# Optimization experiments

Hardware: AMD Instinct MI355X
Metric: run time of the kernel (lower is better)

Reference implementation:

```python
import jax, jax.numpy as jnp
import numpy as np

N = 50000      # nodes
E = 800000     # edges (before self loops)
F = 128        # node_feat_dim
HID = 128      # hidden_dim
LN_EPS = 1e-5
NEG_SLOPE = 0.2


def setup_inputs() -> dict:
    key = jax.random.key(0)
    ks = jax.random.split(key, 32)
    g = lambda k, shape, s=0.05: jax.random.normal(k, shape, dtype=jnp.float32) * s
    inp = {}
    inp["x"] = jax.random.normal(ks[0], (N, F), dtype=jnp.float32)
    inp["edge_index"] = jax.random.randint(ks[1], (2, E), 0, N)
    i = 2
    # conv1: F -> 4 heads x 32, concat -> HID
    inp["W1l"] = g(ks[i], (F, HID)); inp["b1l"] = jnp.zeros((HID,), jnp.float32)
    inp["W1r"] = g(ks[i+1], (F, HID)); inp["b1r"] = jnp.zeros((HID,), jnp.float32)
    inp["a1"] = g(ks[i+2], (4, HID // 4)); inp["c1"] = jnp.zeros((HID,), jnp.float32)
    inp["g1"] = jnp.ones((HID,), jnp.float32); inp["be1"] = jnp.zeros((HID,), jnp.float32)
    # conv2: HID -> 4 heads x 32, concat -> HID
    inp["W2l"] = g(ks[i+3], (HID, HID)); inp["b2l"] = jnp.zeros((HID,), jnp.float32)
    inp["W2r"] = g(ks[i+4], (HID, HID)); inp["b2r"] = jnp.zeros((HID,), jnp.float32)
    inp["a2"] = g(ks[i+5], (4, HID // 4)); inp["c2"] = jnp.zeros((HID,), jnp.float32)
    inp["g2"] = jnp.ones((HID,), jnp.float32); inp["be2"] = jnp.zeros((HID,), jnp.float32)
    # conv3: HID -> 1 head x HID, mean -> HID
    inp["W3l"] = g(ks[i+6], (HID, HID)); inp["b3l"] = jnp.zeros((HID,), jnp.float32)
    inp["W3r"] = g(ks[i+7], (HID, HID)); inp["b3r"] = jnp.zeros((HID,), jnp.float32)
    inp["a3"] = g(ks[i+8], (1, HID)); inp["c3"] = jnp.zeros((HID,), jnp.float32)
    inp["g3"] = jnp.ones((HID,), jnp.float32); inp["be3"] = jnp.zeros((HID,), jnp.float32)
    return inp


def _gatv2(x, Wl, bl, Wr, br, att, bias, src, dst, heads, outc, concat):
    """GATv2Conv: xl=source transform, xr=target transform, edge-wise
    LeakyReLU attention, per-destination segment softmax, scatter-add."""
    n = x.shape[0]
    xl = (x @ Wl + bl).reshape(n, heads, outc)   # lin_l -> source (x_j)
    e_feat = jax.nn.leaky_relu(xl[src] + ((x @ Wr + br).reshape(n, heads, outc))[dst], NEG_SLOPE)  # [E,H,C]
    logits = jnp.einsum('ehc,hc->eh', e_feat, att)                 # [E,H]
    m = jax.ops.segment_max(logits, dst, num_segments=n)           # [N,H]
    a = jnp.exp(logits - m[dst])
    denom = jax.ops.segment_sum(a, dst, num_segments=n)            # [N,H]
    a = a / denom[dst]
    out = jax.ops.segment_sum(xl[src] * a[:, :, None], dst, num_segments=n)  # [N,H,C]
    out = out.reshape(n, heads * outc) if concat else out.mean(axis=1)
    return out + bias


def _ln(h, g, b):
    mu = h.mean(-1, keepdims=True)
    var = ((h - mu) ** 2).mean(-1, keepdims=True)
    return (h - mu) * jax.lax.rsqrt(var + LN_EPS) * g + b


def reference(x, edge_index,
              W1l, b1l, W1r, b1r, a1, c1, g1, be1,
              W2l, b2l, W2r, b2r, a2, c2, g2, be2,
              W3l, b3l, W3r, b3r, a3, c3, g3, be3):
    n = x.shape[0]
    loops = jnp.arange(n, dtype=edge_index.dtype)
    src = jnp.concatenate([edge_index[0], loops])  # add_self_loops=True
    dst = jnp.concatenate([edge_index[1], loops])
    h = _gatv2(x, W1l, b1l, W1r, b1r, a1, c1, src, dst, 4, HID // 4, True)
    h = jax.nn.relu(_ln(h, g1, be1))  # dropout is identity in eval
    h = _gatv2(h, W2l, b2l, W2r, b2r, a2, c2, src, dst, 4, HID // 4, True)
    h = jax.nn.relu(_ln(h, g2, be2))
    h = _gatv2(h, W3l, b3l, W3r, b3r, a3, c3, src, dst, 1, HID, False)
    h = jax.nn.relu(_ln(h, g3, be3))
    return h
```

## Files before the change

kernel.cpp:

```cpp
#include <hip/hip_runtime.h>
#include <hip/hip_bf16.h>


typedef __attribute__((ext_vector_type(8))) short bf16x8;
typedef __attribute__((ext_vector_type(4))) float f32x4;
typedef __attribute__((ext_vector_type(2))) float f32x2;

#define CAP 64

__device__ __forceinline__ ushort f2bf(float f) {
    unsigned u = __float_as_uint(f);
    unsigned r = (u + 0x7fffu + ((u >> 16) & 1u)) >> 16;
    return (ushort)r;
}
__device__ __forceinline__ f32x2 up2(unsigned u) {
    f32x2 r;
    r[0] = __uint_as_float(u << 16);
    r[1] = __uint_as_float(u & 0xffff0000u);
    return r;
}


__global__ __launch_bounds__(256) void prep_kernel(
    const float* __restrict__ x, ushort* __restrict__ xb, int n4,
    const float* W0, const float* W1, const float* W2,
    const float* W3, const float* W4, const float* W5,
    ushort* __restrict__ WT) {
    __shared__ ushort s[128 * 129];
    int tid = threadIdx.x;
    if (blockIdx.x < 6) {
        const float* Ws[6] = {W0, W1, W2, W3, W4, W5};
        const float* W = Ws[blockIdx.x];
        ushort* O = WT + blockIdx.x * 16384;
        for (int r = 0; r < 128; r += 2) {
            int k = r + (tid >> 7);
            int nn = tid & 127;
            s[nn * 129 + k] = f2bf(W[k * 128 + nn]);
        }
        __syncthreads();
        for (int i = tid; i < 16384; i += 256) {
            int nn = i >> 7, k = i & 127;
            O[i] = s[nn * 129 + k];
        }
    } else {
        int i = (blockIdx.x - 6) * 256 + tid;
        if (i >= n4) return;
        float4 v = ((const float4*)x)[i];
        ushort4 o;
        o.x = f2bf(v.x); o.y = f2bf(v.y); o.z = f2bf(v.z); o.w = f2bf(v.w);
        ((ushort4*)xb)[i] = o;
    }
}


__global__ __launch_bounds__(256) void scatter_part_kernel(
    const int* __restrict__ srcrow, const int* __restrict__ dstrow,
    int E, int n, int* __restrict__ cursor, int* __restrict__ srcs) {
    int part = blockIdx.x & 7;
    int sub = blockIdx.x >> 3;
    int nsub = gridDim.x >> 3;
    int ppn = (n + 7) / 8;
    int lo = part * ppn;
    int hi = lo + ppn; if (hi > n) hi = n;
    int ET = E + n;
    int chunk = (ET + nsub - 1) / nsub;
    int s0 = sub * chunk, s1 = s0 + chunk; if (s1 > ET) s1 = ET;
    for (int i = s0 + threadIdx.x; i < s1; i += 256) {
        int d = (i < E) ? dstrow[i] : (i - E);
        if (d >= lo && d < hi) {
            int s = (i < E) ? srcrow[i] : (i - E);
            int pos = atomicAdd(&cursor[d], 1);
            if (pos < CAP) srcs[(d << 6) + pos] = s << 8;
        }
    }
}


__global__ __launch_bounds__(256) void dual_gemm_mfma(
    const ushort* __restrict__ A,
    const ushort* __restrict__ WTl, const ushort* __restrict__ WTr,
    const float* __restrict__ bl, const float* __restrict__ br,
    ushort* __restrict__ XL, ushort* __restrict__ XR, int n) {
    int tid = threadIdx.x;
    int wid = tid >> 6, lane = tid & 63;
    int ln15 = lane & 15, hi = lane >> 4;
    int row0 = blockIdx.x * 64;

    const ushort* WT  = (wid < 2) ? WTl : WTr;
    const float* bias = (wid < 2) ? bl : br;
    ushort* OUT       = (wid < 2) ? XL : XR;
    int colbase = (wid & 1) * 64;

    float bv[4];
    #pragma unroll
    for (int nn = 0; nn < 4; ++nn) bv[nn] = bias[colbase + nn * 16 + ln15];

    f32x4 acc[4][4];
    #pragma unroll
    for (int m = 0; m < 4; ++m)
        #pragma unroll
        for (int nn = 0; nn < 4; ++nn) acc[m][nn] = (f32x4){0.f, 0.f, 0.f, 0.f};

    #pragma unroll
    for (int kk = 0; kk < 4; ++kk) {
        int kb = kk * 64 + hi * 16;
        bf16x8 a[4], b[4];
        #pragma unroll
        for (int m = 0; m < 4; ++m) {
            int r = row0 + m * 16 + ln15;
            a[m] = *(const bf16x8*)((const char*)A + (size_t)r * 256 + kb);
        }
        #pragma unroll
        for (int nn = 0; nn < 4; ++nn) {
            int c = colbase + nn * 16 + ln15;
            b[nn] = *(const bf16x8*)((const char*)WT + (size_t)c * 256 + kb);
        }
        #pragma unroll
        for (int m = 0; m < 4; ++m)
            #pragma unroll
            for (int nn = 0; nn < 4; ++nn)
                acc[m][nn] = __builtin_amdgcn_mfma_f32_16x16x32_bf16(a[m], b[nn], acc[m][nn], 0, 0, 0);
    }

    #pragma unroll
    for (int m = 0; m < 4; ++m) {
        int rbase = row0 + m * 16 + hi * 4;
        bool full = (rbase + 3 < n);
        #pragma unroll
        for (int nn = 0; nn < 4; ++nn) {
            int c = colbase + nn * 16 + ln15;
            ushort* o = OUT + (size_t)rbase * 128 + c;
            float b = bv[nn];
            __hip_bfloat162 h01 = __float22bfloat162_rn(make_float2(acc[m][nn][0] + b, acc[m][nn][1] + b));
            __hip_bfloat162 h23 = __float22bfloat162_rn(make_float2(acc[m][nn][2] + b, acc[m][nn][3] + b));
            ushort2 u01 = *(ushort2*)&h01;
            ushort2 u23 = *(ushort2*)&h23;
            if (full) {
                o[0] = u01.x; o[128] = u01.y; o[256] = u23.x; o[384] = u23.y;
            } else {
                if (rbase + 0 < n) o[0]   = u01.x;
                if (rbase + 1 < n) o[128] = u01.y;
                if (rbase + 2 < n) o[256] = u23.x;
                if (rbase + 3 < n) o[384] = u23.y;
            }
        }
    }
}


template <int GS>
__device__ __forceinline__ void edge_op(uint4 U, const f32x2* xr, const f32x2* at,
                                        f32x2* acc, float& den) {
    f32x2 a0 = up2(U.x), a1 = up2(U.y), a2 = up2(U.z), a3 = up2(U.w);
    f32x2 t = a0 + xr[0];
    t = __builtin_elementwise_max(t, t * 0.2f);
    f32x2 dd = t * at[0];
    t = a1 + xr[1];
    t = __builtin_elementwise_max(t, t * 0.2f);
    dd = __builtin_elementwise_fma(t, at[1], dd);
    t = a2 + xr[2];
    t = __builtin_elementwise_max(t, t * 0.2f);
    dd = __builtin_elementwise_fma(t, at[2], dd);
    t = a3 + xr[3];
    t = __builtin_elementwise_max(t, t * 0.2f);
    dd = __builtin_elementwise_fma(t, at[3], dd);
    float p = dd[0] + dd[1];
    #pragma unroll
    for (int d = 1; d < GS; d <<= 1) p += __shfl_xor(p, d, 64);
    float ew = exp2f(p);
    f32x2 ev; ev[0] = ew; ev[1] = ew;
    acc[0] = __builtin_elementwise_fma(ev, a0, acc[0]);
    acc[1] = __builtin_elementwise_fma(ev, a1, acc[1]);
    acc[2] = __builtin_elementwise_fma(ev, a2, acc[2]);
    acc[3] = __builtin_elementwise_fma(ev, a3, acc[3]);
    den += ew;
}

template <int H, bool OUT_BF16>
__global__ __launch_bounds__(256) void aggregate_kernel(
    const ushort* __restrict__ XL, const ushort* __restrict__ XR,
    const int* __restrict__ deg, const int* __restrict__ srcs,
    const float* __restrict__ att, const float* __restrict__ bias,
    const float* __restrict__ gamma, const float* __restrict__ beta,
    void* __restrict__ OUTP, int n) {
    int tid = threadIdx.x;
    int wid = tid >> 6, lane = tid & 63;
    int g = lane >> 4, l = lane & 15;
    int node = blockIdx.x * 16 + wid * 4 + g;
    bool alive = (node < n);
    int c0 = l * 8;
    constexpr int GS = (128 / H) / 8;

    const char* XLc = (const char*)XL;
    int lb = l * 16;

    f32x2 at[4];
    {
        const float4* ap = (const float4*)(att + c0);
        float4 a0 = ap[0], a1 = ap[1];
        at[0][0] = a0.x; at[0][1] = a0.y; at[1][0] = a0.z; at[1][1] = a0.w;
        at[2][0] = a1.x; at[2][1] = a1.y; at[3][0] = a1.z; at[3][1] = a1.w;
        #pragma unroll
        for (int j = 0; j < 4; ++j) at[j] = at[j] * 1.44269504f;
    }

    f32x2 xr[4];
    int e = 0;
    const int* sp = srcs;
    if (alive) {
        uint4 ur = *(const uint4*)((const char*)XR + ((size_t)node << 8) + lb);
        xr[0] = up2(ur.x); xr[1] = up2(ur.y); xr[2] = up2(ur.z); xr[3] = up2(ur.w);
        e = deg[node]; if (e > CAP) e = CAP;
        sp = srcs + ((size_t)node << 6);
    } else {
        #pragma unroll
        for (int j = 0; j < 4; ++j) { xr[j][0] = 0.f; xr[j][1] = 0.f; }
    }

    f32x2 acc[4];
    #pragma unroll
    for (int j = 0; j < 4; ++j) { acc[j][0] = 0.f; acc[j][1] = 0.f; }
    float den = 0.f;

    int i = 0;
    for (; i + 4 <= e; i += 4) {
        int4 ofs = *(const int4*)(sp + i);
        uint4 u0 = *(const uint4*)(XLc + ofs.x + lb);
        uint4 u1 = *(const uint4*)(XLc + ofs.y + lb);
        uint4 u2 = *(const uint4*)(XLc + ofs.z + lb);
        uint4 u3 = *(const uint4*)(XLc + ofs.w + lb);
        edge_op<GS>(u0, xr, at, acc, den);
        edge_op<GS>(u1, xr, at, acc, den);
        edge_op<GS>(u2, xr, at, acc, den);
        edge_op<GS>(u3, xr, at, acc, den);
    }
    for (; i < e; ++i) {
        uint4 u0 = *(const uint4*)(XLc + sp[i] + lb);
        edge_op<GS>(u0, xr, at, acc, den);
    }

    float inv = 1.f / den;
    f32x2 o[4];
    {
        const f32x2* bp = (const f32x2*)(bias + c0);
        f32x2 iv; iv[0] = inv; iv[1] = inv;
        #pragma unroll
        for (int j = 0; j < 4; ++j) o[j] = __builtin_elementwise_fma(acc[j], iv, bp[j]);
    }

    float ssum = 0.f;
    #pragma unroll
    for (int j = 0; j < 4; ++j) ssum += o[j][0] + o[j][1];
    #pragma unroll
    for (int d = 1; d < 16; d <<= 1) ssum += __shfl_xor(ssum, d, 64);
    float mu = ssum * (1.f / 128.f);
    float vsum = 0.f;
    #pragma unroll
    for (int j = 0; j < 4; ++j) {
        float d0 = o[j][0] - mu, d1 = o[j][1] - mu;
        vsum += d0 * d0 + d1 * d1;
    }
    #pragma unroll
    for (int d = 1; d < 16; d <<= 1) vsum += __shfl_xor(vsum, d, 64);
    float rstd = rsqrtf(vsum * (1.f / 128.f) + 1e-5f);

    if (!alive) return;

    const f32x2* gp = (const f32x2*)(gamma + c0);
    const f32x2* ep = (const f32x2*)(beta + c0);
    float y[8];
    #pragma unroll
    for (int j = 0; j < 4; ++j) {
        f32x2 gj = gp[j], bj = ep[j];
        y[2 * j]     = fmaxf(fmaf((o[j][0] - mu) * rstd, gj[0], bj[0]), 0.f);
        y[2 * j + 1] = fmaxf(fmaf((o[j][1] - mu) * rstd, gj[1], bj[1]), 0.f);
    }

    if (OUT_BF16) {
        __hip_bfloat162 h0 = __float22bfloat162_rn(make_float2(y[0], y[1]));
        __hip_bfloat162 h1 = __float22bfloat162_rn(make_float2(y[2], y[3]));
        __hip_bfloat162 h2 = __float22bfloat162_rn(make_float2(y[4], y[5]));
        __hip_bfloat162 h3 = __float22bfloat162_rn(make_float2(y[6], y[7]));
        uint4 ov;
        ov.x = *(unsigned*)&h0; ov.y = *(unsigned*)&h1;
        ov.z = *(unsigned*)&h2; ov.w = *(unsigned*)&h3;
        *(uint4*)&((ushort*)OUTP)[(size_t)node * 128 + c0] = ov;
    } else {
        float* O = (float*)OUTP + (size_t)node * 128 + c0;
        *(float4*)O = make_float4(y[0], y[1], y[2], y[3]);
        *(float4*)(O + 4) = make_float4(y[4], y[5], y[6], y[7]);
    }
}


extern "C" void kernel_launch(void* const* d_in, const int* in_sizes, int n_in,
                              void* d_out, int out_size, void* d_ws, size_t ws_size,
                              hipStream_t stream) {
    const float* x  = (const float*)d_in[0];
    const int*   ei = (const int*)d_in[1];
    const float *W1l = (const float*)d_in[2],  *b1l = (const float*)d_in[3];
    const float *W1r = (const float*)d_in[4],  *b1r = (const float*)d_in[5];
    const float *a1  = (const float*)d_in[6],  *c1  = (const float*)d_in[7];
    const float *g1  = (const float*)d_in[8],  *be1 = (const float*)d_in[9];
    const float *W2l = (const float*)d_in[10], *b2l = (const float*)d_in[11];
    const float *W2r = (const float*)d_in[12], *b2r = (const float*)d_in[13];
    const float *a2  = (const float*)d_in[14], *c2  = (const float*)d_in[15];
    const float *g2  = (const float*)d_in[16], *be2 = (const float*)d_in[17];
    const float *W3l = (const float*)d_in[18], *b3l = (const float*)d_in[19];
    const float *W3r = (const float*)d_in[20], *b3r = (const float*)d_in[21];
    const float *a3  = (const float*)d_in[22], *c3  = (const float*)d_in[23];
    const float *g3  = (const float*)d_in[24], *be3 = (const float*)d_in[25];

    int n  = in_sizes[0] / 128;
    int E  = in_sizes[1] / 2;
    size_t nPad = (size_t)((n + 63) / 64) * 64;

    char* ws = (char*)d_ws;
    ushort* xb = (ushort*)ws;                      ws += nPad * 128 * 2;
    ushort* XL = (ushort*)ws;                      ws += nPad * 128 * 2;
    ushort* XR = (ushort*)ws;                      ws += nPad * 128 * 2;
    ushort* hb = (ushort*)ws;                      ws += nPad * 128 * 2;
    ushort* WT = (ushort*)ws;                      ws += 6 * 16384 * 2;
    int* cursor = (int*)ws;                        ws += (size_t)n * 4;
    int* srcs   = (int*)ws;

    const int* srcrow = ei;
    const int* dstrow = ei + E;

    int n4 = n * 128 / 4;
    prep_kernel<<<6 + (n4 + 255) / 256, 256, 0, stream>>>(
        x, xb, n4, W1l, W1r, W2l, W2r, W3l, W3r, WT);

    hipMemsetAsync(cursor, 0, (size_t)n * sizeof(int), stream);
    scatter_part_kernel<<<2048, 256, 0, stream>>>(srcrow, dstrow, E, n, cursor, srcs);

    int gb = (int)(nPad / 64);
    int ab = (n + 15) / 16;

    dual_gemm_mfma<<<gb, 256, 0, stream>>>(xb, WT + 0 * 16384, WT + 1 * 16384, b1l, b1r, XL, XR, n);
    aggregate_kernel<4, true><<<ab, 256, 0, stream>>>(XL, XR, cursor, srcs, a1, c1, g1, be1, hb, n);
    dual_gemm_mfma<<<gb, 256, 0, stream>>>(hb, WT + 2 * 16384, WT + 3 * 16384, b2l, b2r, XL, XR, n);
    aggregate_kernel<4, true><<<ab, 256, 0, stream>>>(XL, XR, cursor, srcs, a2, c2, g2, be2, hb, n);
    dual_gemm_mfma<<<gb, 256, 0, stream>>>(hb, WT + 4 * 16384, WT + 5 * 16384, b3l, b3r, XL, XR, n);
    aggregate_kernel<1, false><<<ab, 256, 0, stream>>>(XL, XR, cursor, srcs, a3, c3, g3, be3, d_out, n);
}
```

Before: 368.5 us.

## Split multi-head aggregation per head with node-range partitioning, separate LayerNorm pass

For the two 4-head layers, the fused aggregate+LayerNorm kernel is replaced by a per-head aggregation kernel. Each block handles one head over a contiguous node range, so every gather fetches only a 64-byte slice of XL. This is meant to shrink the gather working set per block and improve cache locality. A separate LayerNorm+ReLU kernel then runs in place on the bf16 output, which adds an extra read/write pass and a launch. The cursor memset is also folded into the prep kernel to drop one API call.

```diff
diff --git a/kernel.cpp b/kernel.cpp
--- a/kernel.cpp
+++ b/kernel.cpp
@@ -25,7 +25,7 @@
     const float* __restrict__ x, ushort* __restrict__ xb, int n4,
     const float* W0, const float* W1, const float* W2,
     const float* W3, const float* W4, const float* W5,
-    ushort* __restrict__ WT) {
+    ushort* __restrict__ WT, int* __restrict__ cursor, int nzb, int n) {
     __shared__ ushort s[128 * 129];
     int tid = threadIdx.x;
     if (blockIdx.x < 6) {
@@ -42,8 +42,16 @@
             int nn = i >> 7, k = i & 127;
             O[i] = s[nn * 129 + k];
         }
+    } else if (blockIdx.x < 6 + nzb) {
+        int base = (blockIdx.x - 6) * 1024 + tid * 4;
+        if (base + 3 < n) {
+            *(int4*)&cursor[base] = make_int4(0, 0, 0, 0);
+        } else {
+            for (int j = 0; j < 4; ++j)
+                if (base + j < n) cursor[base + j] = 0;
+        }
     } else {
-        int i = (blockIdx.x - 6) * 256 + tid;
+        int i = (blockIdx.x - 6 - nzb) * 256 + tid;
         if (i >= n4) return;
         float4 v = ((const float4*)x)[i];
         ushort4 o;
@@ -176,6 +184,153 @@
     den += ew;
 }
 
+
+__global__ __launch_bounds__(256) void agg_head_kernel(
+    const ushort* __restrict__ XL, const ushort* __restrict__ XR,
+    const int* __restrict__ deg, const int* __restrict__ srcs,
+    const float* __restrict__ att, const float* __restrict__ bias,
+    ushort* __restrict__ OUT, int n) {
+    int b = blockIdx.x;
+    int head = (b & 7) >> 1;
+    int s = ((b >> 3) << 1) | (b & 1);
+    int nsub = (gridDim.x >> 3) << 1;
+    int tid = threadIdx.x;
+    int wid = tid >> 6, lane = tid & 63;
+    int ng = lane >> 2;
+    int l4 = lane & 3;
+    int hb = head * 64 + l4 * 16;
+    int c0 = head * 32 + l4 * 8;
+
+    const char* XLc = (const char*)XL;
+
+    f32x2 at[4];
+    {
+        const float4* ap = (const float4*)(att + c0);
+        float4 a0 = ap[0], a1 = ap[1];
+        at[0][0] = a0.x; at[0][1] = a0.y; at[1][0] = a0.z; at[1][1] = a0.w;
+        at[2][0] = a1.x; at[2][1] = a1.y; at[3][0] = a1.z; at[3][1] = a1.w;
+        #pragma unroll
+        for (int j = 0; j < 4; ++j) at[j] = at[j] * 1.44269504f;
+    }
+    f32x2 bi[4];
+    {
+        const f32x2* bp = (const f32x2*)(bias + c0);
+        #pragma unroll
+        for (int j = 0; j < 4; ++j) bi[j] = bp[j];
+    }
+
+    int npb = (n + nsub - 1) / nsub;
+    int v0 = s * npb;
+    int v1 = v0 + npb; if (v1 > n) v1 = n;
+
+    for (int base = v0; base < v1; base += 64) {
+        int node = base + wid * 16 + ng;
+        bool alive = (node < v1);
+
+        f32x2 xr[4];
+        int e = 0;
+        const int* sp = srcs;
+        if (alive) {
+            uint4 ur = *(const uint4*)((const char*)XR + ((size_t)node << 8) + hb);
+            xr[0] = up2(ur.x); xr[1] = up2(ur.y); xr[2] = up2(ur.z); xr[3] = up2(ur.w);
+            e = deg[node]; if (e > CAP) e = CAP;
+            sp = srcs + ((size_t)node << 6);
+        } else {
+            #pragma unroll
+            for (int j = 0; j < 4; ++j) { xr[j][0] = 0.f; xr[j][1] = 0.f; }
+        }
+
+        f32x2 acc[4];
+        #pragma unroll
+        for (int j = 0; j < 4; ++j) { acc[j][0] = 0.f; acc[j][1] = 0.f; }
+        float den = 0.f;
+
+        int i = 0;
+        for (; i + 4 <= e; i += 4) {
+            int4 ofs = *(const int4*)(sp + i);
+            uint4 u0 = *(const uint4*)(XLc + ofs.x + hb);
+            uint4 u1 = *(const uint4*)(XLc + ofs.y + hb);
+            uint4 u2 = *(const uint4*)(XLc + ofs.z + hb);
+            uint4 u3 = *(const uint4*)(XLc + ofs.w + hb);
+            edge_op<4>(u0, xr, at, acc, den);
+            edge_op<4>(u1, xr, at, acc, den);
+            edge_op<4>(u2, xr, at, acc, den);
+            edge_op<4>(u3, xr, at, acc, den);
+        }
+        for (; i < e; ++i) {
+            uint4 u0 = *(const uint4*)(XLc + sp[i] + hb);
+            edge_op<4>(u0, xr, at, acc, den);
+        }
+
+        if (alive) {
+            float inv = 1.f / den;
+            f32x2 iv; iv[0] = inv; iv[1] = inv;
+            uint4 ov;
+            unsigned* op = (unsigned*)&ov;
+            #pragma unroll
+            for (int j = 0; j < 4; ++j) {
+                f32x2 o = __builtin_elementwise_fma(acc[j], iv, bi[j]);
+                __hip_bfloat162 h = __float22bfloat162_rn(make_float2(o[0], o[1]));
+                op[j] = *(unsigned*)&h;
+            }
+            *(uint4*)((char*)OUT + ((size_t)node << 8) + hb) = ov;
+        }
+    }
+}
+
+
+__global__ __launch_bounds__(256) void ln_relu_kernel(
+    ushort* __restrict__ H, const float* __restrict__ gamma,
+    const float* __restrict__ beta, int n) {
+    int tid = threadIdx.x;
+    int wid = tid >> 6, lane = tid & 63;
+    int node = blockIdx.x * 16 + wid * 4 + (lane >> 4);
+    int l = lane & 15, c0 = l * 8;
+    bool alive = (node < n);
+
+    f32x2 o[4];
+    if (alive) {
+        uint4 u = *(const uint4*)&H[(size_t)node * 128 + c0];
+        o[0] = up2(u.x); o[1] = up2(u.y); o[2] = up2(u.z); o[3] = up2(u.w);
+    } else {
+        #pragma unroll
+        for (int j = 0; j < 4; ++j) { o[j][0] = 0.f; o[j][1] = 0.f; }
+    }
+
+    float ssum = 0.f;
+    #pragma unroll
+    for (int j = 0; j < 4; ++j) ssum += o[j][0] + o[j][1];
+    #pragma unroll
+    for (int d = 1; d < 16; d <<= 1) ssum += __shfl_xor(ssum, d, 64);
+    float mu = ssum * (1.f / 128.f);
+    float vsum = 0.f;
+    #pragma unroll
+    for (int j = 0; j < 4; ++j) {
+        float d0 = o[j][0] - mu, d1 = o[j][1] - mu;
+        vsum += d0 * d0 + d1 * d1;
+    }
+    #pragma unroll
+    for (int d = 1; d < 16; d <<= 1) vsum += __shfl_xor(vsum, d, 64);
+    float rstd = rsqrtf(vsum * (1.f / 128.f) + 1e-5f);
+
+    if (!alive) return;
+
+    const f32x2* gp = (const f32x2*)(gamma + c0);
+    const f32x2* ep = (const f32x2*)(beta + c0);
+    uint4 ov;
+    unsigned* op = (unsigned*)&ov;
+    #pragma unroll
+    for (int j = 0; j < 4; ++j) {
+        f32x2 gj = gp[j], bj = ep[j];
+        float y0 = fmaxf(fmaf((o[j][0] - mu) * rstd, gj[0], bj[0]), 0.f);
+        float y1 = fmaxf(fmaf((o[j][1] - mu) * rstd, gj[1], bj[1]), 0.f);
+        __hip_bfloat162 h = __float22bfloat162_rn(make_float2(y0, y1));
+        op[j] = *(unsigned*)&h;
+    }
+    *(uint4*)&H[(size_t)node * 128 + c0] = ov;
+}
+
+
 template <int H, bool OUT_BF16>
 __global__ __launch_bounds__(256) void aggregate_kernel(
     const ushort* __restrict__ XL, const ushort* __restrict__ XR,
@@ -328,19 +483,21 @@
     const int* dstrow = ei + E;
 
     int n4 = n * 128 / 4;
-    prep_kernel<<<6 + (n4 + 255) / 256, 256, 0, stream>>>(
-        x, xb, n4, W1l, W1r, W2l, W2r, W3l, W3r, WT);
-
-    hipMemsetAsync(cursor, 0, (size_t)n * sizeof(int), stream);
+    int nzb = (n + 1023) / 1024;
+    prep_kernel<<<6 + nzb + (n4 + 255) / 256, 256, 0, stream>>>(
+        x, xb, n4, W1l, W1r, W2l, W2r, W3l, W3r, WT, cursor, nzb, n);
+
     scatter_part_kernel<<<2048, 256, 0, stream>>>(srcrow, dstrow, E, n, cursor, srcs);
 
     int gb = (int)(nPad / 64);
     int ab = (n + 15) / 16;
 
     dual_gemm_mfma<<<gb, 256, 0, stream>>>(xb, WT + 0 * 16384, WT + 1 * 16384, b1l, b1r, XL, XR, n);
-    aggregate_kernel<4, true><<<ab, 256, 0, stream>>>(XL, XR, cursor, srcs, a1, c1, g1, be1, hb, n);
+    agg_head_kernel<<<2048, 256, 0, stream>>>(XL, XR, cursor, srcs, a1, c1, hb, n);
+    ln_relu_kernel<<<ab, 256, 0, stream>>>(hb, g1, be1, n);
     dual_gemm_mfma<<<gb, 256, 0, stream>>>(hb, WT + 2 * 16384, WT + 3 * 16384, b2l, b2r, XL, XR, n);
-    aggregate_kernel<4, true><<<ab, 256, 0, stream>>>(XL, XR, cursor, srcs, a2, c2, g2, be2, hb, n);
+    agg_head_kernel<<<2048, 256, 0, stream>>>(XL, XR, cursor, srcs, a2, c2, hb, n);
+    ln_relu_kernel<<<ab, 256, 0, stream>>>(hb, g2, be2, n);
     dual_gemm_mfma<<<gb, 256, 0, stream>>>(hb, WT + 4 * 16384, WT + 5 * 16384, b3l, b3r, XL, XR, n);
     aggregate_kernel<1, false><<<ab, 256, 0, stream>>>(XL, XR, cursor, srcs, a3, c3, g3, be3, d_out, n);
 }
```

New measurement: 413.5 us. 1.12x slower.
